# Kernel tuning notes

Measured on AMD Instinct MI355X. Metric: run time of the kernel, lower is better.

## Reference

```python
import jax, jax.numpy as jnp
import numpy as np

EPS = 1e-5

def layer_norm(x, gamma, beta):
    m = jnp.mean(x, axis=-1, keepdims=True)
    v = jnp.var(x, axis=-1, keepdims=True)
    return (x - m) / jnp.sqrt(v + EPS) * gamma + beta


def setup_inputs() -> dict:
    key = jax.random.key(0)
    ks = jax.random.split(key, 10)
    B, N, D = 2, 2048, 1024
    H, Dh = 16, 64
    C, CD = 256, 512
    inner = H * Dh  # 1024
    J = C + 1 + N  # 2305 = context + null + self

    x = jax.random.normal(ks[0], (B, N, D), dtype=jnp.float32)
    context = jax.random.normal(ks[1], (B, C, CD), dtype=jnp.float32)
    mask = jax.random.uniform(ks[2], (B, C + N)) < 0.9  # bool, mostly True
    attn_bias = jax.random.normal(ks[3], (H, N, J), dtype=jnp.float32) * 0.02

    norm_gamma = jnp.ones((D,), dtype=jnp.float32)
    null_kv = jax.random.normal(ks[4], (2, Dh), dtype=jnp.float32)
    Wq = jax.random.normal(ks[5], (D, inner), dtype=jnp.float32) * (D ** -0.5)
    Wkv = jax.random.normal(ks[6], (D, 2 * Dh), dtype=jnp.float32) * (D ** -0.5)
    ctx_ln_w = jnp.ones((CD,), dtype=jnp.float32)
    ctx_ln_b = jnp.zeros((CD,), dtype=jnp.float32)
    Wctx = jax.random.normal(ks[7], (CD, 2 * Dh), dtype=jnp.float32) * (CD ** -0.5)
    bctx = jnp.zeros((2 * Dh,), dtype=jnp.float32)
    Wout = jax.random.normal(ks[8], (inner, D), dtype=jnp.float32) * (inner ** -0.5)
    out_gamma = jnp.ones((D,), dtype=jnp.float32)

    return {"x": x, "context": context, "mask": mask, "attn_bias": attn_bias,
            "norm_gamma": norm_gamma, "null_kv": null_kv, "Wq": Wq, "Wkv": Wkv,
            "ctx_ln_w": ctx_ln_w, "ctx_ln_b": ctx_ln_b, "Wctx": Wctx, "bctx": bctx,
            "Wout": Wout, "out_gamma": out_gamma}


def reference(x, context, mask, attn_bias, norm_gamma, null_kv, Wq, Wkv,
              ctx_ln_w, ctx_ln_b, Wctx, bctx, Wout, out_gamma):
    B, N, D = x.shape
    Dh = null_kv.shape[-1]
    H = Wq.shape[-1] // Dh
    scale = Dh ** -0.5

    xn = layer_norm(x, norm_gamma, 0.0)
    q = (xn @ Wq).reshape(B, N, H, Dh).transpose(0, 2, 1, 3) * scale  # b h n d
    k, v = jnp.split(xn @ Wkv, 2, axis=-1)  # b n d each (multi-query: shared across heads)

    # prepend learned null kv token
    nk = jnp.broadcast_to(null_kv[0], (B, 1, Dh))
    nv = jnp.broadcast_to(null_kv[1], (B, 1, Dh))
    k = jnp.concatenate([nk, k], axis=1)
    v = jnp.concatenate([nv, v], axis=1)

    # prepend projected context tokens
    cn = layer_norm(context, ctx_ln_w, ctx_ln_b)
    ck, cv = jnp.split(cn @ Wctx + bctx, 2, axis=-1)
    k = jnp.concatenate([ck, k], axis=1)  # b j d, j = C + 1 + N
    v = jnp.concatenate([cv, v], axis=1)

    sim = jnp.einsum('bhid,bjd->bhij', q, k) + attn_bias
    # pad mask with True for the null token (left), then broadcast over h, i
    m = jnp.pad(mask, ((0, 0), (1, 0)), constant_values=True)[:, None, None, :]
    max_neg = -jnp.finfo(sim.dtype).max
    sim = jnp.where(m, sim, max_neg)

    attn = jax.nn.softmax(sim.astype(jnp.float32), axis=-1)
    out = jnp.einsum('bhij,bjd->bhid', attn, v)  # b h n d
    out = out.transpose(0, 2, 1, 3).reshape(B, N, H * Dh)
    return layer_norm(out @ Wout, out_gamma, 0.0)
```

## Files before the change

### kernel.cpp

```cpp
#include <hip/hip_runtime.h>

constexpr int B  = 2;
constexpr int N  = 2048;
constexpr int H  = 16;
constexpr int C  = 256;
constexpr int J  = C + 1 + N;
constexpr int Jp = 2368;
constexpr int NT = Jp / 64;
constexpr float EPS = 1e-5f;

typedef __bf16 bf16x8 __attribute__((ext_vector_type(8)));
typedef float  f32x4  __attribute__((ext_vector_type(4)));
typedef unsigned int uint4v __attribute__((ext_vector_type(4)));
typedef __attribute__((address_space(3))) unsigned int lds_u32;
typedef const __attribute__((address_space(1))) unsigned int glb_u32;

__device__ inline void load_lds16(const void* g, void* l) {
    __builtin_amdgcn_global_load_lds((glb_u32*)g, (lds_u32*)l, 16, 0, 0);
}
__device__ inline unsigned short f2bf(float f) {
    unsigned int u = __builtin_bit_cast(unsigned int, f);
    u += 0x7fffu + ((u >> 16) & 1u);
    return (unsigned short)(u >> 16);
}
__device__ inline unsigned int packbf(float a, float b) {
    return (unsigned int)f2bf(a) | ((unsigned int)f2bf(b) << 16);
}
__device__ inline f32x4 mfma16(bf16x8 a, bf16x8 b, f32x4 c) {
    return __builtin_amdgcn_mfma_f32_16x16x32_bf16(a, b, c, 0, 0, 0);
}

__global__ void mask_prep(const void* __restrict__ mraw, float* __restrict__ maskf) {
    __shared__ int bad_int, bad_f32;
    const int t = threadIdx.x;
    if (t == 0) { bad_int = 0; bad_f32 = 0; }
    __syncthreads();
    const unsigned int* w = (const unsigned int*)mraw;
    int li = 0, lf = 0;
    for (int i = t; i < 1152; i += 256) {
        unsigned int v = w[i];
        if (v > 1u) li = 1;
        if (v != 0u && v != 0x3F800000u) lf = 1;
    }
    if (li) atomicOr(&bad_int, 1);
    if (lf) atomicOr(&bad_f32, 1);
    __syncthreads();
    const int mode = (!bad_int) ? 0 : ((!bad_f32) ? 1 : 2);
    const unsigned char* bytes = (const unsigned char*)mraw;
    for (int i = t; i < 2 * Jp; i += 256) {
        const int b2 = i / Jp, jp = i - b2 * Jp;
        float v;
        if (jp == 0) v = 0.f;
        else if (jp >= J) v = -1e30f;
        else {
            const int idx = b2 * (C + N) + jp - 1;
            const int keep = (mode == 2) ? (bytes[idx] != 0) : (w[idx] != 0u);
            v = keep ? 0.f : -1e30f;
        }
        maskf[i] = v;
    }
}

__global__ void zero_pads(unsigned short* __restrict__ Kb, unsigned short* __restrict__ Vt) {
    const int t = threadIdx.x;
    for (int i = t; i < 2 * 63 * 64; i += 256) {
        const int b2 = i / (63 * 64);
        const int rr = (i / 64) % 63;
        const int d  = i % 64;
        Kb[(size_t)(b2 * Jp + J + rr) * 64 + d] = 0;
    }
    for (int i = t; i < 2 * 64 * 63; i += 256) {
        const int b2 = i / (64 * 63);
        const int d  = (i / 63) % 64;
        const int cc = i % 63;
        Vt[(size_t)(b2 * 64 + d) * Jp + J + cc] = 0;
    }
}

template <int BF16OUT>
__global__ void __launch_bounds__(256) ln1024(const float* __restrict__ x,
                                              const float* __restrict__ gamma,
                                              void* __restrict__ outp) {
    const int row = blockIdx.x;
    const int t = threadIdx.x;
    const float* xr = x + (size_t)row * 1024;
    float4 v = ((const float4*)xr)[t];
    float s  = v.x + v.y + v.z + v.w;
    float ss = v.x * v.x + v.y * v.y + v.z * v.z + v.w * v.w;
    #pragma unroll
    for (int o = 1; o < 64; o <<= 1) {
        s  += __shfl_xor(s, o);
        ss += __shfl_xor(ss, o);
    }
    __shared__ float red[8];
    const int w = t >> 6;
    if ((t & 63) == 0) { red[w * 2] = s; red[w * 2 + 1] = ss; }
    __syncthreads();
    s  = red[0] + red[2] + red[4] + red[6];
    ss = red[1] + red[3] + red[5] + red[7];
    const float mean = s * (1.0f / 1024.0f);
    const float var  = ss * (1.0f / 1024.0f) - mean * mean;
    const float rstd = rsqrtf(var + EPS);
    const float4 g = ((const float4*)gamma)[t];
    float o0 = (v.x - mean) * rstd * g.x;
    float o1 = (v.y - mean) * rstd * g.y;
    float o2 = (v.z - mean) * rstd * g.z;
    float o3 = (v.w - mean) * rstd * g.w;
    if (BF16OUT) {
        ushort4 u;
        u.x = f2bf(o0); u.y = f2bf(o1); u.z = f2bf(o2); u.w = f2bf(o3);
        *(ushort4*)((unsigned short*)outp + (size_t)row * 1024 + t * 4) = u;
    } else {
        *(float4*)((float*)outp + (size_t)row * 1024 + t * 4) = make_float4(o0, o1, o2, o3);
    }
}

__global__ void __launch_bounds__(256) transpose_w(const float* __restrict__ W,
                                                   unsigned short* __restrict__ WT,
                                                   int K, int Nn, float scale) {
    __shared__ float lds[64][68];
    const int k0 = blockIdx.x * 64, n0 = blockIdx.y * 64;
    const int t = threadIdx.x;
    const int kk = t >> 4, nn = (t & 15) * 4;
    #pragma unroll
    for (int r = 0; r < 4; r++) {
        const float4 v = *(const float4*)(W + (size_t)(k0 + kk + r * 16) * Nn + n0 + nn);
        lds[kk + r * 16][nn + 0] = v.x;
        lds[kk + r * 16][nn + 1] = v.y;
        lds[kk + r * 16][nn + 2] = v.z;
        lds[kk + r * 16][nn + 3] = v.w;
    }
    __syncthreads();
    const int nr = t >> 2, kc = (t & 3) * 16;
    #pragma unroll
    for (int u4 = 0; u4 < 4; u4++) {
        ushort4 u;
        u.x = f2bf(lds[kc + u4 * 4 + 0][nr] * scale);
        u.y = f2bf(lds[kc + u4 * 4 + 1][nr] * scale);
        u.z = f2bf(lds[kc + u4 * 4 + 2][nr] * scale);
        u.w = f2bf(lds[kc + u4 * 4 + 3][nr] * scale);
        *(ushort4*)(WT + (size_t)(n0 + nr) * K + k0 + kc + u4 * 4) = u;
    }
}

__global__ void __launch_bounds__(128) ctx_proj(const float* __restrict__ ctx,
                                                const float* __restrict__ lw,
                                                const float* __restrict__ lb,
                                                const float* __restrict__ Wc,
                                                const float* __restrict__ bc,
                                                unsigned short* __restrict__ Kb,
                                                unsigned short* __restrict__ Vt) {
    const int row = blockIdx.x;
    const int b2 = row >> 8, ci = row & 255;
    const int t = threadIdx.x;
    __shared__ float cn[512];
    __shared__ float red[4];
    const float* xr = ctx + (size_t)row * 512;
    float4 v = ((const float4*)xr)[t];
    float s  = v.x + v.y + v.z + v.w;
    float ss = v.x * v.x + v.y * v.y + v.z * v.z + v.w * v.w;
    #pragma unroll
    for (int o = 1; o < 64; o <<= 1) {
        s  += __shfl_xor(s, o);
        ss += __shfl_xor(ss, o);
    }
    const int w = t >> 6;
    if ((t & 63) == 0) { red[w * 2] = s; red[w * 2 + 1] = ss; }
    __syncthreads();
    s  = red[0] + red[2];
    ss = red[1] + red[3];
    const float mean = s * (1.0f / 512.0f);
    const float var  = ss * (1.0f / 512.0f) - mean * mean;
    const float rstd = rsqrtf(var + EPS);
    const float4 g  = ((const float4*)lw)[t];
    const float4 be = ((const float4*)lb)[t];
    float4 c4;
    c4.x = (v.x - mean) * rstd * g.x + be.x;
    c4.y = (v.y - mean) * rstd * g.y + be.y;
    c4.z = (v.z - mean) * rstd * g.z + be.z;
    c4.w = (v.w - mean) * rstd * g.w + be.w;
    *(float4*)&cn[t * 4] = c4;
    __syncthreads();
    float acc = bc[t];
    #pragma unroll 8
    for (int d = 0; d < 512; d++) acc = fmaf(cn[d], Wc[d * 128 + t], acc);
    const unsigned short bv = f2bf(acc);
    if (t < 64) Kb[(size_t)(b2 * Jp + ci) * 64 + t] = bv;
    else        Vt[(size_t)(b2 * 64 + (t - 64)) * Jp + ci] = bv;
}

__global__ void null_fill(const float* __restrict__ nkv,
                          unsigned short* __restrict__ Kb, unsigned short* __restrict__ Vt) {
    const int b2 = blockIdx.x;
    const int t = threadIdx.x;
    Kb[(size_t)(b2 * Jp + 256) * 64 + t] = f2bf(nkv[t]);
    Vt[(size_t)(b2 * 64 + t) * Jp + 256] = f2bf(nkv[64 + t]);
}

template <int MODE>
__global__ void __launch_bounds__(256, 2) gemm_bf16(
        const unsigned short* __restrict__ A, const unsigned short* __restrict__ BT,
        float* __restrict__ Cf, unsigned short* __restrict__ Cb,
        unsigned short* __restrict__ Kb, unsigned short* __restrict__ Vt,
        int M, int Nn, int K) {
    __shared__ __align__(16) unsigned char smem[65536];
    const int t = threadIdx.x;
    const int w = t >> 6, lane = t & 63;
    const int g = lane >> 4, ln15 = lane & 15;
    const int wm = w >> 1, wn = w & 1;
    const int row0 = blockIdx.x * 128, col0 = blockIdx.y * 128;
    const int nk = K >> 6;
    const int ls = lane >> 3;
    const int swz = (lane & 7) ^ ls;

    f32x4 acc[4][4];
    #pragma unroll
    for (int i = 0; i < 4; i++)
        #pragma unroll
        for (int jj = 0; jj < 4; jj++)
            acc[i][jj] = (f32x4){0.f, 0.f, 0.f, 0.f};

    auto stage = [&](int kt, int cur) {
        if (w < 2) {
            const unsigned short* src = A + (size_t)(row0 + w * 64 + ls) * K + kt * 64 + swz * 8;
            unsigned char* dst = smem + cur * 16384 + w * 8192;
            #pragma unroll
            for (int i = 0; i < 8; i++)
                load_lds16(src + (size_t)i * 8 * K, dst + i * 1024);
        } else {
            const unsigned short* src = BT + (size_t)(col0 + (w - 2) * 64 + ls) * K + kt * 64 + swz * 8;
            unsigned char* dst = smem + 32768 + cur * 16384 + (w - 2) * 8192;
            #pragma unroll
            for (int i = 0; i < 8; i++)
                load_lds16(src + (size_t)i * 8 * K, dst + i * 1024);
        }
    };

    stage(0, 0);
    __syncthreads();
    for (int kt = 0; kt < nk; kt++) {
        const int cur = kt & 1;
        if (kt + 1 < nk) stage(kt + 1, cur ^ 1);
        const unsigned char* As = smem + cur * 16384;
        const unsigned char* Bs = smem + 32768 + cur * 16384;
        #pragma unroll
        for (int ks = 0; ks < 2; ks++) {
            bf16x8 af[4], bf[4];
            #pragma unroll
            for (int mq = 0; mq < 4; mq++)
                af[mq] = *(const bf16x8*)(As + (wm * 64 + mq * 16 + ln15) * 128 +
                                          ((ks * 64 + g * 16) ^ ((ln15 & 7) << 4)));
            #pragma unroll
            for (int nq = 0; nq < 4; nq++)
                bf[nq] = *(const bf16x8*)(Bs + (wn * 64 + nq * 16 + ln15) * 128 +
                                          ((ks * 64 + g * 16) ^ ((ln15 & 7) << 4)));
            #pragma unroll
            for (int mq = 0; mq < 4; mq++)
                #pragma unroll
                for (int nq = 0; nq < 4; nq++)
                    acc[mq][nq] = mfma16(af[mq], bf[nq], acc[mq][nq]);
        }
        __syncthreads();
    }

    #pragma unroll
    for (int mq = 0; mq < 4; mq++) {
        #pragma unroll
        for (int nq = 0; nq < 4; nq++) {
            #pragma unroll
            for (int r = 0; r < 4; r++) {
                const int gr = row0 + wm * 64 + mq * 16 + g * 4 + r;
                const int gc = col0 + wn * 64 + nq * 16 + ln15;
                if (MODE == 0) {
                    Cf[(size_t)gr * Nn + gc] = acc[mq][nq][r];
                } else if (MODE == 1) {
                    Cb[(size_t)gr * Nn + gc] = f2bf(acc[mq][nq][r]);
                } else {
                    const int b2 = gr >> 11, tok = gr & 2047;
                    const unsigned short v = f2bf(acc[mq][nq][r]);
                    if (gc < 64) Kb[(size_t)(b2 * Jp + 257 + tok) * 64 + gc] = v;
                    else         Vt[(size_t)(b2 * 64 + gc - 64) * Jp + 257 + tok] = v;
                }
            }
        }
    }
}

__global__ void __launch_bounds__(256, 2) attn_mfma(
        const unsigned short* __restrict__ qb, const unsigned short* __restrict__ Kb,
        const unsigned short* __restrict__ Vt, const float* __restrict__ bias,
        const float* __restrict__ maskf, unsigned short* __restrict__ aout) {
    __shared__ __align__(16) unsigned char smem[65536];
    const int t = threadIdx.x;
    const int w = t >> 6, lane = t & 63;
    const int g = lane >> 4, ln15 = lane & 15;
    const int i0 = blockIdx.x * 64, h = blockIdx.y;
    const int ls = lane >> 3;
    const int swz = (lane & 7) ^ ls;

    auto stage = [&](int jt, int cur) {
        const int j0 = jt * 64;
        const int b2 = w & 1;
        const unsigned short* src;
        size_t sstep;
        if (w < 2) { src = Kb + (size_t)(b2 * Jp + j0 + ls) * 64 + swz * 8; sstep = (size_t)8 * 64; }
        else       { src = Vt + (size_t)(b2 * 64 + ls) * Jp + j0 + swz * 8; sstep = (size_t)8 * Jp; }
        unsigned char* dst = smem + cur * 32768 + w * 8192;
        #pragma unroll
        for (int i = 0; i < 8; i++)
            load_lds16(src + i * sstep, dst + i * 1024);
    };

    bf16x8 qf[2][2];
    #pragma unroll
    for (int b2 = 0; b2 < 2; b2++)
        #pragma unroll
        for (int ks = 0; ks < 2; ks++)
            qf[b2][ks] = *(const bf16x8*)(qb + (size_t)(b2 * N + i0 + w * 16 + ln15) * 1024 +
                                          h * 64 + ks * 32 + g * 8);

    float mrun[2] = {-1e30f, -1e30f};
    float lrun[2] = {0.f, 0.f};
    f32x4 outA[2][4];
    #pragma unroll
    for (int b2 = 0; b2 < 2; b2++)
        #pragma unroll
        for (int nq = 0; nq < 4; nq++)
            outA[b2][nq] = (f32x4){0.f, 0.f, 0.f, 0.f};

    const float* biasRow = bias + ((size_t)h * N + (i0 + w * 16 + ln15)) * J;

    stage(0, 0);
    __syncthreads();

    for (int jt = 0; jt < NT; jt++) {
        const int cur = jt & 1;
        const int j0 = jt * 64;
        if (jt + 1 < NT) stage(jt + 1, cur ^ 1);

        float br[4][4];
        if (jt < NT - 1) {
            #pragma unroll
            for (int jqm = 0; jqm < 4; jqm++)
                #pragma unroll
                for (int rr = 0; rr < 4; rr++)
                    br[jqm][rr] = biasRow[j0 + jqm * 16 + g * 4 + rr];
        } else {
            #pragma unroll
            for (int jqm = 0; jqm < 4; jqm++)
                #pragma unroll
                for (int rr = 0; rr < 4; rr++) {
                    const int jj = j0 + jqm * 16 + g * 4 + rr;
                    br[jqm][rr] = (jj < J) ? biasRow[jj] : 0.f;
                }
        }

        #pragma unroll
        for (int b2 = 0; b2 < 2; b2++) {
            const unsigned char* Kl = smem + cur * 32768 + b2 * 8192;
            const unsigned char* Vl = smem + cur * 32768 + 16384 + b2 * 8192;

            f32x4 mk[4];
            #pragma unroll
            for (int jqm = 0; jqm < 4; jqm++)
                mk[jqm] = *(const f32x4*)(maskf + b2 * Jp + j0 + jqm * 16 + g * 4);

            f32x4 S[4];
            #pragma unroll
            for (int jqm = 0; jqm < 4; jqm++) S[jqm] = (f32x4){0.f, 0.f, 0.f, 0.f};
            #pragma unroll
            for (int ks = 0; ks < 2; ks++) {
                bf16x8 ka[4];
                #pragma unroll
                for (int jqm = 0; jqm < 4; jqm++)
                    ka[jqm] = *(const bf16x8*)(Kl + (jqm * 16 + ln15) * 128 +
                                               ((ks * 64 + g * 16) ^ ((ln15 & 7) << 4)));
                #pragma unroll
                for (int jqm = 0; jqm < 4; jqm++)
                    S[jqm] = mfma16(ka[jqm], qf[b2][ks], S[jqm]);
            }

            float sv[4][4];
            #pragma unroll
            for (int jqm = 0; jqm < 4; jqm++)
                #pragma unroll
                for (int r = 0; r < 4; r++)
                    sv[jqm][r] = S[jqm][r] + br[jqm][r] + mk[jqm][r];

            float tm = -1e30f;
            #pragma unroll
            for (int jqm = 0; jqm < 4; jqm++)
                #pragma unroll
                for (int r = 0; r < 4; r++)
                    tm = fmaxf(tm, sv[jqm][r]);
            tm = fmaxf(tm, __shfl_xor(tm, 16));
            tm = fmaxf(tm, __shfl_xor(tm, 32));
            const float mnew = fmaxf(mrun[b2], tm);
            const float cor = __expf(mrun[b2] - mnew);
            mrun[b2] = mnew;

            float p[4][4];
            float ts = 0.f;
            #pragma unroll
            for (int jqm = 0; jqm < 4; jqm++)
                #pragma unroll
                for (int r = 0; r < 4; r++) {
                    p[jqm][r] = __expf(sv[jqm][r] - mnew);
                    ts += p[jqm][r];
                }
            ts += __shfl_xor(ts, 16);
            ts += __shfl_xor(ts, 32);
            lrun[b2] = lrun[b2] * cor + ts;

            float corr[4];
            #pragma unroll
            for (int r = 0; r < 4; r++) corr[r] = __shfl(cor, g * 4 + r, 64);
            #pragma unroll
            for (int nq = 0; nq < 4; nq++)
                #pragma unroll
                for (int r = 0; r < 4; r++)
                    outA[b2][nq][r] *= corr[r];

            unsigned int Wp[4][2];
            #pragma unroll
            for (int jqm = 0; jqm < 4; jqm++) {
                Wp[jqm][0] = packbf(p[jqm][0], p[jqm][1]);
                Wp[jqm][1] = packbf(p[jqm][2], p[jqm][3]);
            }

            #pragma unroll
            for (int ks = 0; ks < 2; ks++) {
                uint4v wd;
                #pragma unroll
                for (int widx = 0; widx < 4; widx++) {
                    const int srcl = ln15 + (((2 * g + (widx >> 1)) & 3) << 4);
                    const int t0 = __shfl((int)Wp[ks * 2 + 0][widx & 1], srcl, 64);
                    const int t1 = __shfl((int)Wp[ks * 2 + 1][widx & 1], srcl, 64);
                    wd[widx] = (unsigned int)((g >> 1) ? t1 : t0);
                }
                const bf16x8 pa = __builtin_bit_cast(bf16x8, wd);
                #pragma unroll
                for (int nq = 0; nq < 4; nq++) {
                    const bf16x8 vf = *(const bf16x8*)(Vl + (nq * 16 + ln15) * 128 +
                                                       ((ks * 64 + g * 16) ^ ((ln15 & 7) << 4)));
                    outA[b2][nq] = mfma16(pa, vf, outA[b2][nq]);
                }
            }
        }
        __syncthreads();
    }

    #pragma unroll
    for (int b2 = 0; b2 < 2; b2++) {
        const float inv = 1.0f / lrun[b2];
        float invr[4];
        #pragma unroll
        for (int r = 0; r < 4; r++) invr[r] = __shfl(inv, g * 4 + r, 64);
        #pragma unroll
        for (int nq = 0; nq < 4; nq++)
            #pragma unroll
            for (int r = 0; r < 4; r++)
                aout[(size_t)(b2 * N + i0 + w * 16 + g * 4 + r) * 1024 +
                     h * 64 + nq * 16 + ln15] = f2bf(outA[b2][nq][r] * invr[r]);
    }
}

extern "C" void kernel_launch(void* const* d_in, const int* in_sizes, int n_in,
                              void* d_out, int out_size, void* d_ws, size_t ws_size,
                              hipStream_t stream) {
    const float* x         = (const float*)d_in[0];
    const float* context   = (const float*)d_in[1];
    const void*  mask      = d_in[2];
    const float* bias      = (const float*)d_in[3];
    const float* norm_g    = (const float*)d_in[4];
    const float* null_kv   = (const float*)d_in[5];
    const float* Wq        = (const float*)d_in[6];
    const float* Wkv       = (const float*)d_in[7];
    const float* ctx_ln_w  = (const float*)d_in[8];
    const float* ctx_ln_b  = (const float*)d_in[9];
    const float* Wctx      = (const float*)d_in[10];
    const float* bctx      = (const float*)d_in[11];
    const float* Wout      = (const float*)d_in[12];
    const float* out_gamma = (const float*)d_in[13];
    float* out = (float*)d_out;

    unsigned char* wsb = (unsigned char*)d_ws;
    unsigned short* xnb   = (unsigned short*)(wsb + 0);
    unsigned short* qbb   = (unsigned short*)(wsb + 8388608);
    float*          y     = (float*)(wsb + 0);
    unsigned short* aoutp = (unsigned short*)(wsb + 16777216);
    unsigned short* KbP   = (unsigned short*)(wsb + 25165824);
    unsigned short* VtP   = (unsigned short*)(wsb + 25772032);
    float*          maskf = (float*)(wsb + 26378240);
    unsigned short* WqT   = (unsigned short*)(wsb + 26397184);
    unsigned short* WkvT  = (unsigned short*)(wsb + 28494336);
    unsigned short* WoutT = (unsigned short*)(wsb + 28756480);

    mask_prep<<<1, 256, 0, stream>>>(mask, maskf);
    zero_pads<<<1, 256, 0, stream>>>(KbP, VtP);
    ln1024<1><<<B * N, 256, 0, stream>>>(x, norm_g, xnb);
    transpose_w<<<dim3(16, 16), 256, 0, stream>>>(Wq, WqT, 1024, 1024, 0.125f);
    transpose_w<<<dim3(16, 2), 256, 0, stream>>>(Wkv, WkvT, 1024, 128, 1.0f);
    transpose_w<<<dim3(16, 16), 256, 0, stream>>>(Wout, WoutT, 1024, 1024, 1.0f);
    ctx_proj<<<B * C, 128, 0, stream>>>(context, ctx_ln_w, ctx_ln_b, Wctx, bctx, KbP, VtP);
    null_fill<<<B, 64, 0, stream>>>(null_kv, KbP, VtP);
    gemm_bf16<1><<<dim3(32, 8), 256, 0, stream>>>(xnb, WqT, nullptr, qbb, nullptr, nullptr, 4096, 1024, 1024);
    gemm_bf16<2><<<dim3(32, 1), 256, 0, stream>>>(xnb, WkvT, nullptr, nullptr, KbP, VtP, 4096, 128, 1024);
    attn_mfma<<<dim3(32, 16), 256, 0, stream>>>(qbb, KbP, VtP, bias, maskf, aoutp);
    gemm_bf16<0><<<dim3(32, 8), 256, 0, stream>>>(aoutp, WoutT, y, nullptr, nullptr, nullptr, 4096, 1024, 1024);
    ln1024<0><<<B * N, 256, 0, stream>>>(y, out_gamma, out);
}
```

Measured before the change: 274.4 us.

## Drop LDS staging in attention, read K/V from global, use exp2 softmax

The attention kernel no longer stages K and V tiles in shared memory. Each wave now loads its K and V fragments directly from global memory, which relies on the small multi-query K/V staying in cache, and the per-tile block barrier is removed. This frees the 64KB of LDS so launch bounds can rise to 4 blocks per SM. The softmax moves to base 2: LOG2E is folded into the Q weight scale and into the bias, exp2 is issued as raw v_exp_f32, and the output and denominator rescale is skipped when the running max does not change. Smaller changes add s_setprio around the MFMA groups and use native bf16 conversion for packing P, at the cost of more global/L2 traffic per wave.

```diff
diff --git a/kernel.cpp b/kernel.cpp
--- a/kernel.cpp
+++ b/kernel.cpp
@@ -8,6 +8,7 @@
 constexpr int Jp = 2368;
 constexpr int NT = Jp / 64;
 constexpr float EPS = 1e-5f;
+constexpr float LOG2E = 1.4426950408889634f;
 
 typedef __bf16 bf16x8 __attribute__((ext_vector_type(8)));
 typedef float  f32x4  __attribute__((ext_vector_type(4)));
@@ -23,8 +24,16 @@
     u += 0x7fffu + ((u >> 16) & 1u);
     return (unsigned short)(u >> 16);
 }
-__device__ inline unsigned int packbf(float a, float b) {
-    return (unsigned int)f2bf(a) | ((unsigned int)f2bf(b) << 16);
+__device__ inline unsigned int packbf2(float a, float b) {
+    union { __bf16 h[2]; unsigned int u; } cv;
+    cv.h[0] = (__bf16)a;
+    cv.h[1] = (__bf16)b;
+    return cv.u;
+}
+__device__ inline float fexp2(float x) {
+    float r;
+    asm("v_exp_f32 %0, %1" : "=v"(r) : "v"(x));
+    return r;
 }
 __device__ inline f32x4 mfma16(bf16x8 a, bf16x8 b, f32x4 c) {
     return __builtin_amdgcn_mfma_f32_16x16x32_bf16(a, b, c, 0, 0, 0);
@@ -286,30 +295,14 @@
     }
 }
 
-__global__ void __launch_bounds__(256, 2) attn_mfma(
+__global__ void __launch_bounds__(256, 4) attn_v3(
         const unsigned short* __restrict__ qb, const unsigned short* __restrict__ Kb,
         const unsigned short* __restrict__ Vt, const float* __restrict__ bias,
         const float* __restrict__ maskf, unsigned short* __restrict__ aout) {
-    __shared__ __align__(16) unsigned char smem[65536];
     const int t = threadIdx.x;
     const int w = t >> 6, lane = t & 63;
     const int g = lane >> 4, ln15 = lane & 15;
     const int i0 = blockIdx.x * 64, h = blockIdx.y;
-    const int ls = lane >> 3;
-    const int swz = (lane & 7) ^ ls;
-
-    auto stage = [&](int jt, int cur) {
-        const int j0 = jt * 64;
-        const int b2 = w & 1;
-        const unsigned short* src;
-        size_t sstep;
-        if (w < 2) { src = Kb + (size_t)(b2 * Jp + j0 + ls) * 64 + swz * 8; sstep = (size_t)8 * 64; }
-        else       { src = Vt + (size_t)(b2 * 64 + ls) * Jp + j0 + swz * 8; sstep = (size_t)8 * Jp; }
-        unsigned char* dst = smem + cur * 32768 + w * 8192;
-        #pragma unroll
-        for (int i = 0; i < 8; i++)
-            load_lds16(src + i * sstep, dst + i * 1024);
-    };
 
     bf16x8 qf[2][2];
     #pragma unroll
@@ -329,14 +322,11 @@
             outA[b2][nq] = (f32x4){0.f, 0.f, 0.f, 0.f};
 
     const float* biasRow = bias + ((size_t)h * N + (i0 + w * 16 + ln15)) * J;
-
-    stage(0, 0);
-    __syncthreads();
+    const int srclA = ln15 + (((2 * g + 0) & 3) << 4);
+    const int srclB = ln15 + (((2 * g + 1) & 3) << 4);
 
     for (int jt = 0; jt < NT; jt++) {
-        const int cur = jt & 1;
         const int j0 = jt * 64;
-        if (jt + 1 < NT) stage(jt + 1, cur ^ 1);
 
         float br[4][4];
         if (jt < NT - 1) {
@@ -357,8 +347,8 @@
 
         #pragma unroll
         for (int b2 = 0; b2 < 2; b2++) {
-            const unsigned char* Kl = smem + cur * 32768 + b2 * 8192;
-            const unsigned char* Vl = smem + cur * 32768 + 16384 + b2 * 8192;
+            const unsigned short* Kbase = Kb + (size_t)b2 * Jp * 64;
+            const unsigned short* Vbase = Vt + (size_t)b2 * 64 * Jp;
 
             f32x4 mk[4];
             #pragma unroll
@@ -373,11 +363,13 @@
                 bf16x8 ka[4];
                 #pragma unroll
                 for (int jqm = 0; jqm < 4; jqm++)
-                    ka[jqm] = *(const bf16x8*)(Kl + (jqm * 16 + ln15) * 128 +
-                                               ((ks * 64 + g * 16) ^ ((ln15 & 7) << 4)));
+                    ka[jqm] = *(const bf16x8*)(Kbase +
+                              (size_t)(j0 + jqm * 16 + ln15) * 64 + ks * 32 + g * 8);
+                __builtin_amdgcn_s_setprio(1);
                 #pragma unroll
                 for (int jqm = 0; jqm < 4; jqm++)
                     S[jqm] = mfma16(ka[jqm], qf[b2][ks], S[jqm]);
+                __builtin_amdgcn_s_setprio(0);
             }
 
             float sv[4][4];
@@ -385,7 +377,7 @@
             for (int jqm = 0; jqm < 4; jqm++)
                 #pragma unroll
                 for (int r = 0; r < 4; r++)
-                    sv[jqm][r] = S[jqm][r] + br[jqm][r] + mk[jqm][r];
+                    sv[jqm][r] = fmaf(br[jqm][r], LOG2E, S[jqm][r]) + mk[jqm][r];
 
             float tm = -1e30f;
             #pragma unroll
@@ -395,9 +387,22 @@
                     tm = fmaxf(tm, sv[jqm][r]);
             tm = fmaxf(tm, __shfl_xor(tm, 16));
             tm = fmaxf(tm, __shfl_xor(tm, 32));
-            const float mnew = fmaxf(mrun[b2], tm);
-            const float cor = __expf(mrun[b2] - mnew);
-            mrun[b2] = mnew;
+
+            if (!__all(tm <= mrun[b2])) {
+                const float mnew = fmaxf(mrun[b2], tm);
+                const float cor = fexp2(mrun[b2] - mnew);
+                mrun[b2] = mnew;
+                float corr[4];
+                #pragma unroll
+                for (int r = 0; r < 4; r++) corr[r] = __shfl(cor, g * 4 + r, 64);
+                #pragma unroll
+                for (int nq = 0; nq < 4; nq++)
+                    #pragma unroll
+                    for (int r = 0; r < 4; r++)
+                        outA[b2][nq][r] *= corr[r];
+                lrun[b2] *= cor;
+            }
+            const float mcur = mrun[b2];
 
             float p[4][4];
             float ts = 0.f;
@@ -405,27 +410,18 @@
             for (int jqm = 0; jqm < 4; jqm++)
                 #pragma unroll
                 for (int r = 0; r < 4; r++) {
-                    p[jqm][r] = __expf(sv[jqm][r] - mnew);
+                    p[jqm][r] = fexp2(sv[jqm][r] - mcur);
                     ts += p[jqm][r];
                 }
             ts += __shfl_xor(ts, 16);
             ts += __shfl_xor(ts, 32);
-            lrun[b2] = lrun[b2] * cor + ts;
-
-            float corr[4];
-            #pragma unroll
-            for (int r = 0; r < 4; r++) corr[r] = __shfl(cor, g * 4 + r, 64);
-            #pragma unroll
-            for (int nq = 0; nq < 4; nq++)
-                #pragma unroll
-                for (int r = 0; r < 4; r++)
-                    outA[b2][nq][r] *= corr[r];
+            lrun[b2] += ts;
 
             unsigned int Wp[4][2];
             #pragma unroll
             for (int jqm = 0; jqm < 4; jqm++) {
-                Wp[jqm][0] = packbf(p[jqm][0], p[jqm][1]);
-                Wp[jqm][1] = packbf(p[jqm][2], p[jqm][3]);
+                Wp[jqm][0] = packbf2(p[jqm][0], p[jqm][1]);
+                Wp[jqm][1] = packbf2(p[jqm][2], p[jqm][3]);
             }
 
             #pragma unroll
@@ -433,21 +429,24 @@
                 uint4v wd;
                 #pragma unroll
                 for (int widx = 0; widx < 4; widx++) {
-                    const int srcl = ln15 + (((2 * g + (widx >> 1)) & 3) << 4);
+                    const int srcl = (widx >> 1) ? srclB : srclA;
                     const int t0 = __shfl((int)Wp[ks * 2 + 0][widx & 1], srcl, 64);
                     const int t1 = __shfl((int)Wp[ks * 2 + 1][widx & 1], srcl, 64);
                     wd[widx] = (unsigned int)((g >> 1) ? t1 : t0);
                 }
                 const bf16x8 pa = __builtin_bit_cast(bf16x8, wd);
-                #pragma unroll
-                for (int nq = 0; nq < 4; nq++) {
-                    const bf16x8 vf = *(const bf16x8*)(Vl + (nq * 16 + ln15) * 128 +
-                                                       ((ks * 64 + g * 16) ^ ((ln15 & 7) << 4)));
-                    outA[b2][nq] = mfma16(pa, vf, outA[b2][nq]);
-                }
+                bf16x8 vf[4];
+                #pragma unroll
+                for (int nq = 0; nq < 4; nq++)
+                    vf[nq] = *(const bf16x8*)(Vbase +
+                             (size_t)(nq * 16 + ln15) * Jp + j0 + ks * 32 + g * 8);
+                __builtin_amdgcn_s_setprio(1);
+                #pragma unroll
+                for (int nq = 0; nq < 4; nq++)
+                    outA[b2][nq] = mfma16(pa, vf[nq], outA[b2][nq]);
+                __builtin_amdgcn_s_setprio(0);
             }
         }
-        __syncthreads();
     }
 
     #pragma unroll
@@ -499,14 +498,14 @@
     mask_prep<<<1, 256, 0, stream>>>(mask, maskf);
     zero_pads<<<1, 256, 0, stream>>>(KbP, VtP);
     ln1024<1><<<B * N, 256, 0, stream>>>(x, norm_g, xnb);
-    transpose_w<<<dim3(16, 16), 256, 0, stream>>>(Wq, WqT, 1024, 1024, 0.125f);
+    transpose_w<<<dim3(16, 16), 256, 0, stream>>>(Wq, WqT, 1024, 1024, 0.125f * LOG2E);
     transpose_w<<<dim3(16, 2), 256, 0, stream>>>(Wkv, WkvT, 1024, 128, 1.0f);
     transpose_w<<<dim3(16, 16), 256, 0, stream>>>(Wout, WoutT, 1024, 1024, 1.0f);
     ctx_proj<<<B * C, 128, 0, stream>>>(context, ctx_ln_w, ctx_ln_b, Wctx, bctx, KbP, VtP);
     null_fill<<<B, 64, 0, stream>>>(null_kv, KbP, VtP);
     gemm_bf16<1><<<dim3(32, 8), 256, 0, stream>>>(xnb, WqT, nullptr, qbb, nullptr, nullptr, 4096, 1024, 1024);
     gemm_bf16<2><<<dim3(32, 1), 256, 0, stream>>>(xnb, WkvT, nullptr, nullptr, KbP, VtP, 4096, 128, 1024);
-    attn_mfma<<<dim3(32, 16), 256, 0, stream>>>(qbb, KbP, VtP, bias, maskf, aoutp);
+    attn_v3<<<dim3(32, 16), 256, 0, stream>>>(qbb, KbP, VtP, bias, maskf, aoutp);
     gemm_bf16<0><<<dim3(32, 8), 256, 0, stream>>>(aoutp, WoutT, y, nullptr, nullptr, nullptr, 4096, 1024, 1024);
     ln1024<0><<<B * N, 256, 0, stream>>>(y, out_gamma, out);
 }
```

Result: slower. 479.4 us (+74.7%).
